# Kernel optimization log

Measured on AMD Instinct MI355X. Metric: run time of the kernel, lower is better.

## Reference

```python
import jax, jax.numpy as jnp
import numpy as np

SEQ = 2048
DIM = 512
HEADS = 8
DH = DIM // HEADS
EPS = float(np.finfo(np.float32).eps)
NEG = float(np.finfo(np.float32).max)


def _pos_encoding(seq, dim):
    idx = jnp.arange(seq, dtype=jnp.float32)
    div = 1.0 / (10000.0 ** (jnp.arange(0, dim, 2, dtype=jnp.float32) / dim) + EPS)
    ang = idx[:, None] * div[None, :]  # [S, dim/2]
    pos = jnp.zeros((seq, dim), dtype=jnp.float32)
    pos = pos.at[:, 0::2].set(jnp.sin(ang)).at[:, 1::2].set(jnp.cos(ang))
    return pos[None]  # [1, S, D]


def _rmsnorm(x, gain, bias):
    d = x.shape[-1]
    scale = jnp.linalg.norm(x, axis=-1, keepdims=True) * (d ** -0.5)
    return x / (scale + EPS) * gain + bias


def setup_inputs() -> dict:
    key = jax.random.key(0)
    ks = jax.random.split(key, 12)
    s = 0.02
    return {
        "x": jax.random.normal(ks[0], (4, SEQ, DIM), dtype=jnp.float32),
        "norm1_g": jnp.ones((DIM,), jnp.float32),
        "norm1_b": jnp.zeros((DIM,), jnp.float32),
        "wq": jax.random.normal(ks[1], (DIM, DIM), jnp.float32) * s,
        "wk": jax.random.normal(ks[2], (DIM, DIM), jnp.float32) * s,
        "wv": jax.random.normal(ks[3], (DIM, DIM), jnp.float32) * s,
        "wo": jax.random.normal(ks[4], (DIM, DIM), jnp.float32) * s,
        "norm2_g": jnp.ones((DIM,), jnp.float32),
        "norm2_b": jnp.zeros((DIM,), jnp.float32),
        "ff_w1": jax.random.normal(ks[5], (DIM, DIM), jnp.float32) * s,
        "ff_b1": jnp.zeros((DIM,), jnp.float32),
        "ffn_g": jnp.ones((DIM,), jnp.float32),
        "ffn_b": jnp.zeros((DIM,), jnp.float32),
        "sw_w": jax.random.normal(ks[6], (2 * DIM, DIM), jnp.float32) * s,
        "sw_b": jnp.zeros((2 * DIM,), jnp.float32),
        "ff_w2": jax.random.normal(ks[7], (DIM, DIM), jnp.float32) * s,
        "ff_b2": jnp.zeros((DIM,), jnp.float32),
    }


def _block(x, norm1_g, norm1_b, wq, wk, wv, wo, norm2_g, norm2_b,
           ff_w1, ff_b1, ffn_g, ffn_b, sw_w, sw_b, ff_w2, ff_b2):
    B = x.shape[0]
    x = x + _pos_encoding(SEQ, DIM)

    # --- multi-head attention on RMSNorm(x) ---
    h = _rmsnorm(x, norm1_g, norm1_b)
    q = (h @ wq.T).reshape(B, SEQ, HEADS, DH).transpose(0, 2, 1, 3)  # [B,H,S,Dh]
    k = (h @ wk.T).reshape(B, SEQ, HEADS, DH).transpose(0, 2, 1, 3)
    v = (h @ wv.T).reshape(B, SEQ, HEADS, DH).transpose(0, 2, 1, 3)
    scores = jnp.einsum("bhqd,bhkd->bhqk", q, k)  # materialized [B,H,S,S]
    causal_mask = jnp.triu(jnp.ones((SEQ, SEQ), dtype=bool), k=1)
    scores = jnp.where(causal_mask[None, None], -NEG, scores)
    # NOTE: original scales by dim_k**-0.5 = dim_emb**-0.5 (not head dim)
    attn = jax.nn.softmax(scores * (DIM ** -0.5), axis=-1)
    o = jnp.einsum("bhqk,bhkd->bhqd", attn, v)
    o = o.transpose(0, 2, 1, 3).reshape(B, SEQ, DIM) @ wo.T
    x = x + o

    # --- feed-forward: Linear -> RMSNorm -> SwiGLU -> Linear ---
    h = _rmsnorm(x, norm2_g, norm2_b)
    h = h @ ff_w1.T + ff_b1
    h = _rmsnorm(h, ffn_g, ffn_b)
    u = h @ sw_w.T + sw_b  # [B,S,2*DIM]
    h = jax.nn.silu(u[..., :DIM]) + u[..., DIM:]
    h = h @ ff_w2.T + ff_b2
    return x + h


def reference(x, norm1_g, norm1_b, wq, wk, wv, wo, norm2_g, norm2_b,
              ff_w1, ff_b1, ffn_g, ffn_b, sw_w, sw_b, ff_w2, ff_b2):
    return _block(x, norm1_g, norm1_b, wq, wk, wv, wo, norm2_g, norm2_b,
                  ff_w1, ff_b1, ffn_g, ffn_b, sw_w, sw_b, ff_w2, ff_b2)
```

## Files before the change

### kernel.cpp

```cpp
#include <hip/hip_runtime.h>
#include <hip/hip_bf16.h>
#include <cstdint>
#include <cstddef>

typedef __bf16 bf16;
typedef __bf16 bf16x4_t __attribute__((ext_vector_type(4)));
typedef __bf16 bf16x8_t __attribute__((ext_vector_type(8)));
typedef float f32x4 __attribute__((ext_vector_type(4)));
typedef float f32x16 __attribute__((ext_vector_type(16)));

#define DEV_INLINE __device__ __forceinline__

constexpr int SEQ = 2048, DIM = 512, HEADS = 8, DH = 64;
constexpr int ROWS = 4 * SEQ;
constexpr float EPSF = 1.1920928955078125e-07f;
constexpr float RSQRT_DIM = 0.04419417382415922f;
constexpr float LOG2E = 1.44269504088896f;

DEV_INLINE void load_lds16(const void* g, void* l) {
  __builtin_amdgcn_global_load_lds(
      (const __attribute__((address_space(1))) void*)g,
      (__attribute__((address_space(3))) void*)l,
      16, 0, 0);
}

DEV_INLINE unsigned int packbf(float a, float b) {
  union { unsigned int u; bf16 h[2]; } z;
  z.h[0] = (bf16)a;
  z.h[1] = (bf16)b;
  return z.u;
}

DEV_INLINE void permswap(unsigned int& a, unsigned int& b) {
  asm volatile("v_permlane32_swap_b32 %0, %1" : "+v"(a), "+v"(b));
}

__global__ __launch_bounds__(256) void cvt_all_k(
    const float* __restrict__ wq, const float* __restrict__ wk,
    const float* __restrict__ wv, const float* __restrict__ wo,
    const float* __restrict__ w1, const float* __restrict__ sww,
    const float* __restrict__ w2, bf16* __restrict__ dst) {
  const int i = blockIdx.x * 256 + threadIdx.x;
  const float* src;
  int local;
  if (i < 196608)      { src = (i < 65536) ? wq : (i < 131072) ? wk : wv; local = i & 65535; }
  else if (i < 262144) { src = wo;  local = i - 196608; }
  else if (i < 327680) { src = w1;  local = i - 262144; }
  else if (i < 458752) { src = sww; local = i - 327680; }
  else                 { src = w2;  local = i - 458752; }
  float4 f = reinterpret_cast<const float4*>(src)[local];
  bf16x4_t o;
  o[0] = (bf16)f.x; o[1] = (bf16)f.y; o[2] = (bf16)f.z; o[3] = (bf16)f.w;
  reinterpret_cast<bf16x4_t*>(dst)[i] = o;
}

template <bool ADDPOS>
__global__ __launch_bounds__(256) void rmsnorm_k(const float* __restrict__ in,
                                                 const float* __restrict__ gain,
                                                 const float* __restrict__ bias,
                                                 float* __restrict__ outF,
                                                 bf16* __restrict__ outB) {
  const int sub = threadIdx.x >> 7;
  const int row = blockIdx.x * 2 + sub;
  const int t = threadIdx.x & 127;
  const float* rp = in + (size_t)row * DIM;
  float4 v = reinterpret_cast<const float4*>(rp)[t];
  if constexpr (ADDPOS) {
    const int s = row & (SEQ - 1);
    const float e0 = (float)(4 * t) * (1.0f / (float)DIM);
    const float e1 = (float)(4 * t + 2) * (1.0f / (float)DIM);
    const float d0 = 1.0f / (powf(10000.0f, e0) + EPSF);
    const float d1 = 1.0f / (powf(10000.0f, e1) + EPSF);
    const float a0 = (float)s * d0, a1 = (float)s * d1;
    v.x += sinf(a0); v.y += cosf(a0);
    v.z += sinf(a1); v.w += cosf(a1);
  }
  float ss = v.x * v.x + v.y * v.y + v.z * v.z + v.w * v.w;
#pragma unroll
  for (int off = 32; off > 0; off >>= 1) ss += __shfl_down(ss, off, 64);
  __shared__ float red[4];
  const int wv = threadIdx.x >> 6;
  if ((threadIdx.x & 63) == 0) red[wv] = ss;
  __syncthreads();
  const float total = red[sub * 2] + red[sub * 2 + 1];
  const float scale = sqrtf(total) * RSQRT_DIM;
  const float inv = 1.0f / (scale + EPSF);
  if constexpr (ADDPOS)
    reinterpret_cast<float4*>(outF + (size_t)row * DIM)[t] = v;
  const float4 g = reinterpret_cast<const float4*>(gain)[t];
  const float4 bb = reinterpret_cast<const float4*>(bias)[t];
  bf16x4_t o;
  o[0] = (bf16)(v.x * inv * g.x + bb.x);
  o[1] = (bf16)(v.y * inv * g.y + bb.y);
  o[2] = (bf16)(v.z * inv * g.z + bb.z);
  o[3] = (bf16)(v.w * inv * g.w + bb.w);
  reinterpret_cast<bf16x4_t*>(outB + (size_t)row * DIM)[t] = o;
}

enum { MODE_QKV = 0, MODE_RES = 1, MODE_BIAS = 2, MODE_SWIGLU2 = 3, MODE_RESBIAS = 4 };

template <int MODE>
__global__ __launch_bounds__(256) void gemm_bt_k(
    const bf16* __restrict__ A, const bf16* __restrict__ Bt,
    const float* __restrict__ bias, const float* __restrict__ res,
    float* __restrict__ outF, bf16* __restrict__ outB,
    bf16* __restrict__ oq, bf16* __restrict__ okk, bf16* __restrict__ ovT) {
  constexpr int BELEMS = (MODE == MODE_SWIGLU2) ? 4096 : 2048;
  __shared__ __align__(16) bf16 sA[4][128 * 32];
  __shared__ __align__(16) bf16 sB[4][BELEMS];
  const int tid = threadIdx.x;
  const int wave = tid >> 6, lane = tid & 63;
  const int m0 = blockIdx.x * 128, n0 = blockIdx.y * 64;
  const int wm = wave >> 1, wn = wave & 1;
  const int lr = lane & 15, lk = (lane >> 4) * 8;

  const f32x4 fzero = {0.f, 0.f, 0.f, 0.f};
  f32x4 acc[4][2], acc2[4][2];
#pragma unroll
  for (int i = 0; i < 4; ++i)
#pragma unroll
    for (int j = 0; j < 2; ++j) { acc[i][j] = fzero; acc2[i][j] = fzero; }

  const int off0 = wave * 1024 + lane * 16;
  const int rowS = off0 >> 6, colb = off0 & 63;

  auto stage = [&](int buf, int kt) {
    const int k0 = kt * 32;
    load_lds16((const char*)A + ((size_t)(m0 + rowS) * 512 + k0) * 2 + colb,
               (char*)&sA[buf][0] + off0);
    load_lds16((const char*)A + ((size_t)(m0 + 64 + rowS) * 512 + k0) * 2 + colb,
               (char*)&sA[buf][0] + 4096 + off0);
    load_lds16((const char*)Bt + ((size_t)(n0 + rowS) * 512 + k0) * 2 + colb,
               (char*)&sB[buf][0] + off0);
    if constexpr (MODE == MODE_SWIGLU2)
      load_lds16((const char*)Bt + ((size_t)(512 + n0 + rowS) * 512 + k0) * 2 + colb,
                 (char*)&sB[buf][0] + 4096 + off0);
  };

  stage(0, 0);
  stage(1, 1);
  stage(2, 2);
  if constexpr (MODE == MODE_SWIGLU2)
    asm volatile("s_waitcnt vmcnt(8)\ns_barrier" ::: "memory");
  else
    asm volatile("s_waitcnt vmcnt(6)\ns_barrier" ::: "memory");

#pragma unroll
  for (int kt = 0; kt < 16; ++kt) {
    const int cur = kt & 3;
    if (kt + 3 < 16) stage((kt + 3) & 3, kt + 3);
    bf16x8_t af[4], bfr[2], bfr2[2];
#pragma unroll
    for (int mf = 0; mf < 4; ++mf)
      af[mf] = *(const bf16x8_t*)(&sA[cur][0] + (wm * 64 + mf * 16 + lr) * 32 + lk);
#pragma unroll
    for (int nf = 0; nf < 2; ++nf)
      bfr[nf] = *(const bf16x8_t*)(&sB[cur][0] + (wn * 32 + nf * 16 + lr) * 32 + lk);
    if constexpr (MODE == MODE_SWIGLU2) {
#pragma unroll
      for (int nf = 0; nf < 2; ++nf)
        bfr2[nf] = *(const bf16x8_t*)(&sB[cur][0] + 2048 + (wn * 32 + nf * 16 + lr) * 32 + lk);
    }
    asm volatile("s_waitcnt lgkmcnt(0)" ::: "memory");
#pragma unroll
    for (int mf = 0; mf < 4; ++mf)
#pragma unroll
      for (int nf = 0; nf < 2; ++nf) {
        acc[mf][nf] = __builtin_amdgcn_mfma_f32_16x16x32_bf16(af[mf], bfr[nf],
                                                              acc[mf][nf], 0, 0, 0);
        if constexpr (MODE == MODE_SWIGLU2)
          acc2[mf][nf] = __builtin_amdgcn_mfma_f32_16x16x32_bf16(af[mf], bfr2[nf],
                                                                 acc2[mf][nf], 0, 0, 0);
      }
    if (kt < 13) {
      if constexpr (MODE == MODE_SWIGLU2)
        asm volatile("s_waitcnt vmcnt(8)\ns_barrier" ::: "memory");
      else
        asm volatile("s_waitcnt vmcnt(6)\ns_barrier" ::: "memory");
    } else if (kt == 13) {
      if constexpr (MODE == MODE_SWIGLU2)
        asm volatile("s_waitcnt vmcnt(4)\ns_barrier" ::: "memory");
      else
        asm volatile("s_waitcnt vmcnt(3)\ns_barrier" ::: "memory");
    } else if (kt == 14) {
      asm volatile("s_waitcnt vmcnt(0)\ns_barrier" ::: "memory");
    }
  }

  if constexpr (MODE == MODE_QKV) {
    const int which = n0 >> 9;
    const int h = (n0 >> 6) & 7;
    const int b = m0 >> 11;
    const int s0tok = m0 & 2047;
    bf16* st = &sA[0][0];
    const int rb = wm * 64 + (lane >> 4) * 4;
    const int cb = wn * 32 + lr;
    __syncthreads();
    if (which < 2) {
#pragma unroll
      for (int mf = 0; mf < 4; ++mf)
#pragma unroll
        for (int nf = 0; nf < 2; ++nf)
#pragma unroll
          for (int rg = 0; rg < 4; ++rg) {
            float v = acc[mf][nf][rg];
            if (which == 0) v *= RSQRT_DIM * LOG2E;
            st[(rb + mf * 16 + rg) * 72 + cb + nf * 16] = (bf16)v;
          }
      __syncthreads();
      bf16* dst = which == 0 ? oq : okk;
#pragma unroll
      for (int j = 0; j < 4; ++j) {
        const int flat = j * 4096 + tid * 16;
        const int row = flat >> 7, offb = flat & 127;
        bf16x8_t vv = *(const bf16x8_t*)(st + row * 72 + offb / 2);
        const size_t addr =
            ((size_t)((b * HEADS + h) * SEQ + s0tok + row)) * DH + offb / 2;
        *(bf16x8_t*)(dst + addr) = vv;
      }
    } else {
#pragma unroll
      for (int mf = 0; mf < 4; ++mf)
#pragma unroll
        for (int nf = 0; nf < 2; ++nf)
#pragma unroll
          for (int rg = 0; rg < 4; ++rg)
            st[(cb + nf * 16) * 136 + rb + mf * 16 + rg] = (bf16)acc[mf][nf][rg];
      __syncthreads();
#pragma unroll
      for (int j = 0; j < 4; ++j) {
        const int flat = j * 4096 + tid * 16;
        const int row = flat >> 8, offb = flat & 255;
        bf16x8_t vv = *(const bf16x8_t*)(st + row * 136 + offb / 2);
        const size_t addr =
            ((size_t)((b * HEADS + h) * DH + row)) * SEQ + s0tok + offb / 2;
        *(bf16x8_t*)(ovT + addr) = vv;
      }
    }
    return;
  }

  const int rbase = m0 + wm * 64 + (lane >> 4) * 4;
  const int cbase = n0 + wn * 32 + lr;
#pragma unroll
  for (int mf = 0; mf < 4; ++mf) {
#pragma unroll
    for (int nf = 0; nf < 2; ++nf) {
      const int c = cbase + nf * 16;
#pragma unroll
      for (int rg = 0; rg < 4; ++rg) {
        const int r = rbase + mf * 16 + rg;
        float v = acc[mf][nf][rg];
        if constexpr (MODE == MODE_RES) {
          const size_t idx = (size_t)r * 512 + c;
          outF[idx] = res[idx] + v;
        } else if constexpr (MODE == MODE_BIAS) {
          const size_t idx = (size_t)r * 512 + c;
          outF[idx] = v + bias[c];
        } else if constexpr (MODE == MODE_SWIGLU2) {
          const size_t idx = (size_t)r * 512 + c;
          const float u1 = v + bias[c];
          const float u2 = acc2[mf][nf][rg] + bias[512 + c];
          const float sig = 1.0f / (1.0f + __expf(-u1));
          outB[idx] = (bf16)(u1 * sig + u2);
        } else {
          const size_t idx = (size_t)r * 512 + c;
          outF[idx] = res[idx] + v + bias[c];
        }
      }
    }
  }
}

__global__ __launch_bounds__(256)
__attribute__((amdgpu_waves_per_eu(2)))
void attn_k(const bf16* __restrict__ Q,
            const bf16* __restrict__ K,
            const bf16* __restrict__ VT,
            bf16* __restrict__ O) {
  const int tid = threadIdx.x;
  const int wave = tid >> 6, lane = tid & 63;
  const int lq = lane & 31, hi = lane >> 5;

  const int wg = blockIdx.x;
  const int xcd = wg & 7;
  const int bh = xcd * 4 + ((wg >> 3) & 3);
  const int qi = (wg < 256) ? (15 - (wg >> 5)) : ((wg - 256) >> 5);
  const int qb = qi * 128;
  const int qw = qb + wave * 32;
  const int NT = qi * 2 + 2;
  const int nkt = qi * 2 + 1 + (wave >> 1);

  const char* Kg = (const char*)(K + (size_t)bh * SEQ * DH);
  const char* Vg = (const char*)(VT + (size_t)bh * DH * SEQ);
  const bf16* Qp = Q + (size_t)bh * SEQ * DH;

  __shared__ __align__(16) bf16 smem[6][4096];

  bf16x8_t qf[4];
  {
    const bf16* qp = Qp + (size_t)(qw + lq) * DH + 8 * hi;
    qf[0] = *(const bf16x8_t*)(qp);
    qf[1] = *(const bf16x8_t*)(qp + 16);
    qf[2] = *(const bf16x8_t*)(qp + 32);
    qf[3] = *(const bf16x8_t*)(qp + 48);
  }

  const int slot = lane & 7, rsub = lane >> 3;
  const int sgoff = (slot * 16) ^ (rsub << 4);

  auto stage = [&](int buf, int kt) {
#pragma unroll
    for (int c = 0; c < 2; ++c) {
      const int row = c * 32 + wave * 8 + rsub;
      const int ldsb = c * 4096 + wave * 1024 + lane * 16;
      load_lds16(Kg + (size_t)(kt * 64 + row) * 128 + sgoff,
                 (char*)&smem[buf][0] + ldsb);
      load_lds16(Vg + (size_t)row * 4096 + (size_t)kt * 128 + sgoff,
                 (char*)&smem[3 + buf][0] + ldsb);
    }
  };

  stage(0, 0);
  stage(1, 1);
  asm volatile("s_waitcnt vmcnt(4)\ns_barrier" ::: "memory");

  f32x16 oa0, oa1;
#pragma unroll
  for (int r = 0; r < 16; ++r) { oa0[r] = 0.f; oa1[r] = 0.f; }
  float lsum = 0.f;
  const int xorv = (lq & 7) << 4;

  union U8 { unsigned int u[4]; bf16x8_t v; };

  for (int kt = 0; kt < NT; ++kt) {
    const int buf = kt % 3;
    if (kt + 2 < NT) stage((kt + 2) % 3, kt + 2);
    if (kt < nkt) {
      const char* kb = (const char*)&smem[buf][0];
      const char* vb = (const char*)&smem[3 + buf][0];

      f32x16 s0, s1;
#pragma unroll
      for (int r = 0; r < 16; ++r) { s0[r] = 0.f; s1[r] = 0.f; }
      __builtin_amdgcn_s_setprio(1);
#pragma unroll
      for (int s = 0; s < 4; ++s) {
        const int bo = (32 * s + 16 * hi) ^ xorv;
        s0 = __builtin_amdgcn_mfma_f32_32x32x16_bf16(
            *(const bf16x8_t*)(kb + lq * 128 + bo), qf[s], s0, 0, 0, 0);
        s1 = __builtin_amdgcn_mfma_f32_32x32x16_bf16(
            *(const bf16x8_t*)(kb + (32 + lq) * 128 + bo), qf[s], s1, 0, 0, 0);
      }
      __builtin_amdgcn_s_setprio(0);

      if (kt == nkt - 1) {
        const int qg = qw + lq;
#pragma unroll
        for (int r = 0; r < 16; ++r) {
          const int kl = kt * 64 + (r & 3) + 8 * (r >> 2) + 4 * hi;
          if (kl > qg) s0[r] = -3.0e38f;
          if (kl + 32 > qg) s1[r] = -3.0e38f;
        }
      }

#pragma unroll
      for (int r = 0; r < 16; ++r) {
        const float a = exp2f(s0[r]); s0[r] = a; lsum += a;
        const float b = exp2f(s1[r]); s1[r] = b; lsum += b;
      }

      U8 p00, p01, p10, p11;
      {
        unsigned int x0, x1, y0, y1;
        x0 = packbf(s0[0], s0[1]);  x1 = packbf(s0[4], s0[5]);
        y0 = packbf(s0[2], s0[3]);  y1 = packbf(s0[6], s0[7]);
        permswap(x0, x1); permswap(y0, y1);
        p00.u[0] = x0; p00.u[2] = x1; p00.u[1] = y0; p00.u[3] = y1;
        x0 = packbf(s0[8], s0[9]);   x1 = packbf(s0[12], s0[13]);
        y0 = packbf(s0[10], s0[11]); y1 = packbf(s0[14], s0[15]);
        permswap(x0, x1); permswap(y0, y1);
        p01.u[0] = x0; p01.u[2] = x1; p01.u[1] = y0; p01.u[3] = y1;
        x0 = packbf(s1[0], s1[1]);  x1 = packbf(s1[4], s1[5]);
        y0 = packbf(s1[2], s1[3]);  y1 = packbf(s1[6], s1[7]);
        permswap(x0, x1); permswap(y0, y1);
        p10.u[0] = x0; p10.u[2] = x1; p10.u[1] = y0; p10.u[3] = y1;
        x0 = packbf(s1[8], s1[9]);   x1 = packbf(s1[12], s1[13]);
        y0 = packbf(s1[10], s1[11]); y1 = packbf(s1[14], s1[15]);
        permswap(x0, x1); permswap(y0, y1);
        p11.u[0] = x0; p11.u[2] = x1; p11.u[1] = y0; p11.u[3] = y1;
      }

      __builtin_amdgcn_s_setprio(1);
      {
        const int b0 = (16 * hi) ^ xorv;
        const int b1 = (32 + 16 * hi) ^ xorv;
        const int b2 = (64 + 16 * hi) ^ xorv;
        const int b3 = (96 + 16 * hi) ^ xorv;
        oa0 = __builtin_amdgcn_mfma_f32_32x32x16_bf16(
            *(const bf16x8_t*)(vb + lq * 128 + b0), p00.v, oa0, 0, 0, 0);
        oa0 = __builtin_amdgcn_mfma_f32_32x32x16_bf16(
            *(const bf16x8_t*)(vb + lq * 128 + b1), p01.v, oa0, 0, 0, 0);
        oa0 = __builtin_amdgcn_mfma_f32_32x32x16_bf16(
            *(const bf16x8_t*)(vb + lq * 128 + b2), p10.v, oa0, 0, 0, 0);
        oa0 = __builtin_amdgcn_mfma_f32_32x32x16_bf16(
            *(const bf16x8_t*)(vb + lq * 128 + b3), p11.v, oa0, 0, 0, 0);
        oa1 = __builtin_amdgcn_mfma_f32_32x32x16_bf16(
            *(const bf16x8_t*)(vb + (32 + lq) * 128 + b0), p00.v, oa1, 0, 0, 0);
        oa1 = __builtin_amdgcn_mfma_f32_32x32x16_bf16(
            *(const bf16x8_t*)(vb + (32 + lq) * 128 + b1), p01.v, oa1, 0, 0, 0);
        oa1 = __builtin_amdgcn_mfma_f32_32x32x16_bf16(
            *(const bf16x8_t*)(vb + (32 + lq) * 128 + b2), p10.v, oa1, 0, 0, 0);
        oa1 = __builtin_amdgcn_mfma_f32_32x32x16_bf16(
            *(const bf16x8_t*)(vb + (32 + lq) * 128 + b3), p11.v, oa1, 0, 0, 0);
      }
      __builtin_amdgcn_s_setprio(0);
    }
    if (kt + 2 < NT)
      asm volatile("s_waitcnt vmcnt(4)\ns_barrier" ::: "memory");
    else
      asm volatile("s_waitcnt vmcnt(0)\ns_barrier" ::: "memory");
  }

  const float lrun = lsum + __shfl_xor(lsum, 32);
  const float inv = 1.0f / lrun;
  bf16* ol = &smem[0][0] + wave * 2560;
#pragma unroll
  for (int t4 = 0; t4 < 4; ++t4) {
    const int d0 = 8 * t4 + 4 * hi;
    *(unsigned int*)(ol + lq * 80 + d0)          = packbf(oa0[4 * t4] * inv, oa0[4 * t4 + 1] * inv);
    *(unsigned int*)(ol + lq * 80 + d0 + 2)      = packbf(oa0[4 * t4 + 2] * inv, oa0[4 * t4 + 3] * inv);
    *(unsigned int*)(ol + lq * 80 + 32 + d0)     = packbf(oa1[4 * t4] * inv, oa1[4 * t4 + 1] * inv);
    *(unsigned int*)(ol + lq * 80 + 32 + d0 + 2) = packbf(oa1[4 * t4 + 2] * inv, oa1[4 * t4 + 3] * inv);
  }
  const int b = bh >> 3, h = bh & 7;
#pragma unroll
  for (int ps = 0; ps < 4; ++ps) {
    const int flat = ps * 1024 + lane * 16;
    const int qr = flat >> 7, off = flat & 127;
    bf16x8_t vv = *(const bf16x8_t*)((const char*)ol + qr * 160 + off);
    *(bf16x8_t*)(O + ((size_t)(b * SEQ + qw + qr)) * DIM + h * 64 + off / 2) = vv;
  }
}

extern "C" void kernel_launch(void* const* d_in, const int* in_sizes, int n_in,
                              void* d_out, int out_size, void* d_ws, size_t ws_size,
                              hipStream_t stream) {
  const float* x   = (const float*)d_in[0];
  const float* n1g = (const float*)d_in[1];
  const float* n1b = (const float*)d_in[2];
  const float* wq  = (const float*)d_in[3];
  const float* wk  = (const float*)d_in[4];
  const float* wv  = (const float*)d_in[5];
  const float* wo  = (const float*)d_in[6];
  const float* n2g = (const float*)d_in[7];
  const float* n2b = (const float*)d_in[8];
  const float* w1  = (const float*)d_in[9];
  const float* b1  = (const float*)d_in[10];
  const float* ffg = (const float*)d_in[11];
  const float* ffb = (const float*)d_in[12];
  const float* sww = (const float*)d_in[13];
  const float* swb = (const float*)d_in[14];
  const float* w2  = (const float*)d_in[15];
  const float* b2  = (const float*)d_in[16];
  float* out = (float*)d_out;

  char* ws = (char*)d_ws;
  float* x1 = (float*)(ws + 0);
  float* x2 = (float*)(ws + 16777216);
  bf16* hbuf   = (bf16*)(ws + 33554432);
  bf16* qbuf   = (bf16*)(ws + 41943040);
  bf16* kbuf   = (bf16*)(ws + 50331648);
  bf16* vtbuf  = (bf16*)(ws + 58720256);
  bf16* obuf   = (bf16*)(ws + 67108864);
  bf16* wbase  = (bf16*)(ws + 75497472);
  bf16* wqkv_b = wbase;
  bf16* wo_b   = wbase + 786432;
  bf16* w1_b   = wbase + 1048576;
  bf16* sw_b16 = wbase + 1310720;
  bf16* w2_b   = wbase + 1835008;

  cvt_all_k<<<2048, 256, 0, stream>>>(wq, wk, wv, wo, w1, sww, w2, wbase);

  rmsnorm_k<true><<<ROWS / 2, 256, 0, stream>>>(x, n1g, n1b, x1, hbuf);

  gemm_bt_k<MODE_QKV><<<dim3(64, 24), 256, 0, stream>>>(
      hbuf, wqkv_b, nullptr, nullptr, nullptr, nullptr, qbuf, kbuf, vtbuf);

  attn_k<<<512, 256, 0, stream>>>(qbuf, kbuf, vtbuf, obuf);

  gemm_bt_k<MODE_RES><<<dim3(64, 8), 256, 0, stream>>>(
      obuf, wo_b, nullptr, x1, x2, nullptr, nullptr, nullptr, nullptr);

  rmsnorm_k<false><<<ROWS / 2, 256, 0, stream>>>(x2, n2g, n2b, nullptr, hbuf);

  gemm_bt_k<MODE_BIAS><<<dim3(64, 8), 256, 0, stream>>>(
      hbuf, w1_b, b1, nullptr, x1, nullptr, nullptr, nullptr, nullptr);

  rmsnorm_k<false><<<ROWS / 2, 256, 0, stream>>>(x1, ffg, ffb, nullptr, hbuf);

  gemm_bt_k<MODE_SWIGLU2><<<dim3(64, 8), 256, 0, stream>>>(
      hbuf, sw_b16, swb, nullptr, nullptr, qbuf, nullptr, nullptr, nullptr);

  gemm_bt_k<MODE_RESBIAS><<<dim3(64, 8), 256, 0, stream>>>(
      qbuf, w2_b, b2, x2, out, nullptr, nullptr, nullptr, nullptr);
}
```

Before: 158.4 us.

## Split long causal attention query blocks across two workgroups with merge kernel

Query blocks 8-15 of the causal attention, which have the most key tiles, are now split along the key dimension into two workgroups. Each half writes unnormalised fp32 partial outputs and row sums to scratch space reused from x2 and hbuf. A new merge kernel adds the halves and normalises them into the bf16 output. The goal is to even out per-workgroup work and shorten the tail of the 512-block grid, at the cost of extra scratch traffic and one more kernel launch. The softmax sum is also split into four accumulators to shorten the dependency chain.

```diff
diff --git a/kernel.cpp b/kernel.cpp
--- a/kernel.cpp
+++ b/kernel.cpp
@@ -272,12 +272,19 @@
   }
 }
 
+__constant__ int kSlot[24] = {
+  7 | 0,  15 | 16, 15 | 32, 14 | 16, 14 | 32, 6 | 0,  13 | 16, 13 | 32,
+  12 | 16, 12 | 32, 5 | 0,  11 | 16, 11 | 32, 10 | 16, 10 | 32, 4 | 0,
+  9 | 16, 9 | 32,  8 | 16,  8 | 32,  3 | 0,  2 | 0,  1 | 0,  0 | 0};
+
 __global__ __launch_bounds__(256)
 __attribute__((amdgpu_waves_per_eu(2)))
 void attn_k(const bf16* __restrict__ Q,
             const bf16* __restrict__ K,
             const bf16* __restrict__ VT,
-            bf16* __restrict__ O) {
+            bf16* __restrict__ O,
+            float* __restrict__ scrO,
+            float* __restrict__ scrL) {
   const int tid = threadIdx.x;
   const int wave = tid >> 6, lane = tid & 63;
   const int lq = lane & 31, hi = lane >> 5;
@@ -285,11 +292,13 @@
   const int wg = blockIdx.x;
   const int xcd = wg & 7;
   const int bh = xcd * 4 + ((wg >> 3) & 3);
-  const int qi = (wg < 256) ? (15 - (wg >> 5)) : ((wg - 256) >> 5);
-  const int qb = qi * 128;
-  const int qw = qb + wave * 32;
-  const int NT = qi * 2 + 2;
-  const int nkt = qi * 2 + 1 + (wave >> 1);
+  const int enc = kSlot[wg >> 5];
+  const int qi = enc & 15;
+  const int mode = enc >> 4;
+  const int qw = qi * 128 + wave * 32;
+  const int kt0 = (mode == 2) ? (qi + 1) : 0;
+  const int ktEnd = (mode == 1) ? (qi + 1) : (2 * qi + 2);
+  const int nkt = (mode == 1) ? ktEnd : (2 * qi + 1 + (wave >> 1));
 
   const char* Kg = (const char*)(K + (size_t)bh * SEQ * DH);
   const char* Vg = (const char*)(VT + (size_t)bh * DH * SEQ);
@@ -321,21 +330,22 @@
     }
   };
 
-  stage(0, 0);
-  stage(1, 1);
+  stage(0, kt0);
+  stage(1, kt0 + 1);
   asm volatile("s_waitcnt vmcnt(4)\ns_barrier" ::: "memory");
 
   f32x16 oa0, oa1;
 #pragma unroll
   for (int r = 0; r < 16; ++r) { oa0[r] = 0.f; oa1[r] = 0.f; }
-  float lsum = 0.f;
+  float ls0 = 0.f, ls1 = 0.f, ls2 = 0.f, ls3 = 0.f;
   const int xorv = (lq & 7) << 4;
 
   union U8 { unsigned int u[4]; bf16x8_t v; };
 
-  for (int kt = 0; kt < NT; ++kt) {
-    const int buf = kt % 3;
-    if (kt + 2 < NT) stage((kt + 2) % 3, kt + 2);
+  for (int kt = kt0; kt < ktEnd; ++kt) {
+    const int rel = kt - kt0;
+    const int buf = rel % 3;
+    if (kt + 2 < ktEnd) stage((rel + 2) % 3, kt + 2);
     if (kt < nkt) {
       const char* kb = (const char*)&smem[buf][0];
       const char* vb = (const char*)&smem[3 + buf][0];
@@ -354,7 +364,7 @@
       }
       __builtin_amdgcn_s_setprio(0);
 
-      if (kt == nkt - 1) {
+      if (mode != 1 && kt == nkt - 1) {
         const int qg = qw + lq;
 #pragma unroll
         for (int r = 0; r < 16; ++r) {
@@ -365,9 +375,14 @@
       }
 
 #pragma unroll
-      for (int r = 0; r < 16; ++r) {
-        const float a = exp2f(s0[r]); s0[r] = a; lsum += a;
-        const float b = exp2f(s1[r]); s1[r] = b; lsum += b;
+      for (int r = 0; r < 8; ++r) {
+        const float a = exp2f(s0[r]); s0[r] = a; ls0 += a;
+        const float b = exp2f(s1[r]); s1[r] = b; ls2 += b;
+      }
+#pragma unroll
+      for (int r = 8; r < 16; ++r) {
+        const float a = exp2f(s0[r]); s0[r] = a; ls1 += a;
+        const float b = exp2f(s1[r]); s1[r] = b; ls3 += b;
       }
 
       U8 p00, p01, p10, p11;
@@ -416,31 +431,71 @@
       }
       __builtin_amdgcn_s_setprio(0);
     }
-    if (kt + 2 < NT)
+    if (kt + 2 < ktEnd)
       asm volatile("s_waitcnt vmcnt(4)\ns_barrier" ::: "memory");
     else
       asm volatile("s_waitcnt vmcnt(0)\ns_barrier" ::: "memory");
   }
 
-  const float lrun = lsum + __shfl_xor(lsum, 32);
-  const float inv = 1.0f / lrun;
-  bf16* ol = &smem[0][0] + wave * 2560;
-#pragma unroll
-  for (int t4 = 0; t4 < 4; ++t4) {
-    const int d0 = 8 * t4 + 4 * hi;
-    *(unsigned int*)(ol + lq * 80 + d0)          = packbf(oa0[4 * t4] * inv, oa0[4 * t4 + 1] * inv);
-    *(unsigned int*)(ol + lq * 80 + d0 + 2)      = packbf(oa0[4 * t4 + 2] * inv, oa0[4 * t4 + 3] * inv);
-    *(unsigned int*)(ol + lq * 80 + 32 + d0)     = packbf(oa1[4 * t4] * inv, oa1[4 * t4 + 1] * inv);
-    *(unsigned int*)(ol + lq * 80 + 32 + d0 + 2) = packbf(oa1[4 * t4 + 2] * inv, oa1[4 * t4 + 3] * inv);
-  }
-  const int b = bh >> 3, h = bh & 7;
-#pragma unroll
-  for (int ps = 0; ps < 4; ++ps) {
-    const int flat = ps * 1024 + lane * 16;
-    const int qr = flat >> 7, off = flat & 127;
-    bf16x8_t vv = *(const bf16x8_t*)((const char*)ol + qr * 160 + off);
-    *(bf16x8_t*)(O + ((size_t)(b * SEQ + qw + qr)) * DIM + h * 64 + off / 2) = vv;
-  }
+  const float l4 = (ls0 + ls1) + (ls2 + ls3);
+
+  if (mode == 0) {
+    const float lrun = l4 + __shfl_xor(l4, 32);
+    const float inv = 1.0f / lrun;
+    bf16* ol = &smem[0][0] + wave * 2560;
+#pragma unroll
+    for (int t4 = 0; t4 < 4; ++t4) {
+      const int d0 = 8 * t4 + 4 * hi;
+      *(unsigned int*)(ol + lq * 80 + d0)          = packbf(oa0[4 * t4] * inv, oa0[4 * t4 + 1] * inv);
+      *(unsigned int*)(ol + lq * 80 + d0 + 2)      = packbf(oa0[4 * t4 + 2] * inv, oa0[4 * t4 + 3] * inv);
+      *(unsigned int*)(ol + lq * 80 + 32 + d0)     = packbf(oa1[4 * t4] * inv, oa1[4 * t4 + 1] * inv);
+      *(unsigned int*)(ol + lq * 80 + 32 + d0 + 2) = packbf(oa1[4 * t4 + 2] * inv, oa1[4 * t4 + 3] * inv);
+    }
+    const int b = bh >> 3, h = bh & 7;
+#pragma unroll
+    for (int ps = 0; ps < 4; ++ps) {
+      const int flat = ps * 1024 + lane * 16;
+      const int qr = flat >> 7, off = flat & 127;
+      bf16x8_t vv = *(const bf16x8_t*)((const char*)ol + qr * 160 + off);
+      *(bf16x8_t*)(O + ((size_t)(b * SEQ + qw + qr)) * DIM + h * 64 + off / 2) = vv;
+    }
+  } else {
+    const float lrow = l4 + __shfl_xor(l4, 32);
+    float* so = scrO + ((size_t)(mode - 1) * 256 + bh * 8 + (qi - 8)) * 8192;
+    const int qoff = (wave * 32 + lq) * 64;
+#pragma unroll
+    for (int t4 = 0; t4 < 4; ++t4) {
+      const int d0 = 8 * t4 + 4 * hi;
+      f32x4 w0 = {oa0[4 * t4], oa0[4 * t4 + 1], oa0[4 * t4 + 2], oa0[4 * t4 + 3]};
+      f32x4 w1 = {oa1[4 * t4], oa1[4 * t4 + 1], oa1[4 * t4 + 2], oa1[4 * t4 + 3]};
+      *(f32x4*)(so + qoff + d0) = w0;
+      *(f32x4*)(so + qoff + 32 + d0) = w1;
+    }
+    if (!hi)
+      scrL[(mode - 1) * 32768 + bh * 1024 + (qi - 8) * 128 + wave * 32 + lq] = lrow;
+  }
+}
+
+__global__ __launch_bounds__(256) void attn_merge_k(
+    const float* __restrict__ scrO, const float* __restrict__ scrL,
+    bf16* __restrict__ O) {
+  const int i = blockIdx.x * 256 + threadIdx.x;
+  const int bh = i >> 14;
+  const int rem = i & 16383;
+  const int u = rem >> 4;
+  const int dq = (rem & 15) << 2;
+  const size_t oA = ((size_t)bh * 8 + (u >> 7)) * 8192 + (u & 127) * 64 + dq;
+  const f32x4 a = *(const f32x4*)(scrO + oA);
+  const f32x4 b = *(const f32x4*)(scrO + 2097152 + oA);
+  const float l = scrL[bh * 1024 + u] + scrL[32768 + bh * 1024 + u];
+  const float inv = 1.0f / l;
+  const int bb = bh >> 3, h = bh & 7;
+  bf16x4_t o;
+  o[0] = (bf16)((a[0] + b[0]) * inv);
+  o[1] = (bf16)((a[1] + b[1]) * inv);
+  o[2] = (bf16)((a[2] + b[2]) * inv);
+  o[3] = (bf16)((a[3] + b[3]) * inv);
+  *(bf16x4_t*)(O + ((size_t)(bb * SEQ + 1024 + u)) * DIM + h * 64 + dq) = o;
 }
 
 extern "C" void kernel_launch(void* const* d_in, const int* in_sizes, int n_in,
@@ -479,6 +534,8 @@
   bf16* w1_b   = wbase + 1048576;
   bf16* sw_b16 = wbase + 1310720;
   bf16* w2_b   = wbase + 1835008;
+  float* scrO  = (float*)x2;
+  float* scrL  = (float*)hbuf;
 
   cvt_all_k<<<2048, 256, 0, stream>>>(wq, wk, wv, wo, w1, sww, w2, wbase);
 
@@ -487,7 +544,8 @@
   gemm_bt_k<MODE_QKV><<<dim3(64, 24), 256, 0, stream>>>(
       hbuf, wqkv_b, nullptr, nullptr, nullptr, nullptr, qbuf, kbuf, vtbuf);
 
-  attn_k<<<512, 256, 0, stream>>>(qbuf, kbuf, vtbuf, obuf);
+  attn_k<<<768, 256, 0, stream>>>(qbuf, kbuf, vtbuf, obuf, scrO, scrL);
+  attn_merge_k<<<2048, 256, 0, stream>>>(scrO, scrL, obuf);
 
   gemm_bt_k<MODE_RES><<<dim3(64, 8), 256, 0, stream>>>(
       obuf, wo_b, nullptr, x1, x2, nullptr, nullptr, nullptr, nullptr);
```

Result: no change. 157.5 us (-0.6%).
